# Optimization experiments

Hardware: AMD Instinct MI355X
Metric: run time of the kernel (lower is better)

The kernel has to match this reference:

```python
import jax, jax.numpy as jnp
import numpy as np

NUM_HEADS = 8

def setup_inputs() -> dict:
    key = jax.random.key(0)
    k1, k2, k3, k4 = jax.random.split(key, 4)
    B, N, C = 2, 4096, 768
    x = jax.random.normal(k1, (B, N, C), dtype=jnp.float32)
    w_qkv = jax.random.normal(k2, (C, 3 * C), dtype=jnp.float32) * (C ** -0.5)
    w_proj = jax.random.normal(k3, (C, C), dtype=jnp.float32) * (C ** -0.5)
    b_proj = jax.random.normal(k4, (C,), dtype=jnp.float32) * 0.02
    return {"x": x, "w_qkv": w_qkv, "w_proj": w_proj, "b_proj": b_proj}

def reference(x, w_qkv, w_proj, b_proj):
    B, N, C = x.shape
    H = NUM_HEADS
    Dh = C // H
    scale = Dh ** -0.5
    # qkv: [B, N, 3C] -> [B, N, 3, H, Dh] -> [3, B, H, N, Dh]
    qkv = (x @ w_qkv).reshape(B, N, 3, H, Dh).transpose(2, 0, 3, 1, 4)
    q, k, v = qkv[0], qkv[1], qkv[2]
    attn = jnp.einsum('bhqd,bhkd->bhqk', q, k) * scale  # [B,H,N,N]
    attn = jax.nn.softmax(attn, axis=-1)
    out = jnp.einsum('bhqk,bhkd->bhqd', attn, v)        # [B,H,N,Dh]
    out = out.transpose(0, 2, 1, 3).reshape(B, N, C)
    return out @ w_proj + b_proj
```

## Files before the change

kernel.cpp:

```cpp
#include <hip/hip_runtime.h>
#include <hip/hip_bf16.h>

typedef __attribute__((ext_vector_type(8))) short short8;
typedef __attribute__((ext_vector_type(4))) short short4v;
typedef __attribute__((ext_vector_type(4))) float f32x4;
typedef __attribute__((ext_vector_type(16))) float f32x16;

#define MFMA16(a,b,c) __builtin_amdgcn_mfma_f32_16x16x32_bf16(a,b,c,0,0,0)
#define MFMA32(a,b,c) __builtin_amdgcn_mfma_f32_32x32x16_bf16(a,b,c,0,0,0)

__device__ __forceinline__ unsigned short f2b_rne(float f){
  union { float f; unsigned int u; } v; v.f = f;
  unsigned int u = v.u;
  return (unsigned short)((u + 0x7FFFu + ((u >> 16) & 1u)) >> 16);
}

__device__ __forceinline__ f32x16 zero16(){
  f32x16 z;
  #pragma unroll
  for (int i = 0; i < 16; ++i) z[i] = 0.f;
  return z;
}

__global__ __launch_bounds__(256) void k_cvt(const float* __restrict__ in,
                                             unsigned short* __restrict__ out, int n8){
  int i = blockIdx.x * 256 + threadIdx.x;
  if (i >= n8) return;
  const float4* p = (const float4*)in + (size_t)i * 2;
  float4 a = p[0], b = p[1];
  short8 o;
  o[0] = (short)f2b_rne(a.x); o[1] = (short)f2b_rne(a.y);
  o[2] = (short)f2b_rne(a.z); o[3] = (short)f2b_rne(a.w);
  o[4] = (short)f2b_rne(b.x); o[5] = (short)f2b_rne(b.y);
  o[6] = (short)f2b_rne(b.z); o[7] = (short)f2b_rne(b.w);
  *((short8*)out + i) = o;
}

__global__ void k_transpose_cvt(const float* __restrict__ in, unsigned short* __restrict__ out,
                                int R, int Cc){
  __shared__ unsigned short tile[32][33];
  int c0 = blockIdx.x * 32, r0 = blockIdx.y * 32;
  int tx = threadIdx.x, ty = threadIdx.y;
  #pragma unroll
  for (int i = 0; i < 32; i += 8)
    tile[ty + i][tx] = f2b_rne(in[(size_t)(r0 + ty + i) * Cc + c0 + tx]);
  __syncthreads();
  #pragma unroll
  for (int i = 0; i < 32; i += 8)
    out[(size_t)(c0 + ty + i) * R + r0 + tx] = tile[tx][ty + i];
}

__global__ __launch_bounds__(256) void k_gemm_qkv(
    const unsigned short* __restrict__ A,
    const unsigned short* __restrict__ Bt,
    unsigned short* __restrict__ qbuf,
    unsigned short* __restrict__ kbuf,
    unsigned short* __restrict__ vtb)
{
  __shared__ short As[128 * 40];
  __shared__ short Bs[128 * 40];
  int m0 = blockIdx.x * 128, n0 = blockIdx.y * 128;
  int t = threadIdx.x, l = t & 63, w = t >> 6;
  int lr = l & 15, lh = l >> 4;
  int wr = w >> 1, wc = w & 1;

  int row0 = t >> 2, cs0 = t & 3;
  int row1 = row0 + 64;
  const unsigned short* ga0 = A  + (size_t)(m0 + row0) * 768 + cs0 * 8;
  const unsigned short* ga1 = A  + (size_t)(m0 + row1) * 768 + cs0 * 8;
  const unsigned short* gb0 = Bt + (size_t)(n0 + row0) * 768 + cs0 * 8;
  const unsigned short* gb1 = Bt + (size_t)(n0 + row1) * 768 + cs0 * 8;
  short* la0 = As + row0 * 40 + cs0 * 8;
  short* la1 = As + row1 * 40 + cs0 * 8;
  short* lb0 = Bs + row0 * 40 + cs0 * 8;
  short* lb1 = Bs + row1 * 40 + cs0 * 8;

  f32x4 acc[4][4];
  f32x4 z4 = {0.f, 0.f, 0.f, 0.f};
  #pragma unroll
  for (int mf = 0; mf < 4; ++mf)
    #pragma unroll
    for (int nf = 0; nf < 4; ++nf) acc[mf][nf] = z4;

  short8 ra0 = *(const short8*)ga0;
  short8 ra1 = *(const short8*)ga1;
  short8 rb0 = *(const short8*)gb0;
  short8 rb1 = *(const short8*)gb1;

  for (int kt = 0; kt < 24; ++kt){
    __syncthreads();
    *(short8*)la0 = ra0; *(short8*)la1 = ra1;
    *(short8*)lb0 = rb0; *(short8*)lb1 = rb1;
    __syncthreads();
    if (kt < 23){
      ra0 = *(const short8*)(ga0 + (kt + 1) * 32);
      ra1 = *(const short8*)(ga1 + (kt + 1) * 32);
      rb0 = *(const short8*)(gb0 + (kt + 1) * 32);
      rb1 = *(const short8*)(gb1 + (kt + 1) * 32);
    }
    short8 af[4], bfm[4];
    #pragma unroll
    for (int mf = 0; mf < 4; ++mf)
      af[mf] = *(const short8*)(As + (wr * 64 + mf * 16 + lr) * 40 + lh * 8);
    #pragma unroll
    for (int nf = 0; nf < 4; ++nf)
      bfm[nf] = *(const short8*)(Bs + (wc * 64 + nf * 16 + lr) * 40 + lh * 8);
    #pragma unroll
    for (int mf = 0; mf < 4; ++mf)
      #pragma unroll
      for (int nf = 0; nf < 4; ++nf)
        acc[mf][nf] = MFMA16(af[mf], bfm[nf], acc[mf][nf]);
  }

  const float qscale = 0.10206207261596577f * 1.4426950408889634f;
  int three = n0 / 768;
  int b_ = m0 >> 12;
  int ntok0 = m0 & 4095;
  #pragma unroll
  for (int nf = 0; nf < 4; ++nf){
    int gcol = n0 + wc * 64 + nf * 16 + lr;
    int jj = gcol - three * 768;
    int h = jj / 96;
    int dh = jj - h * 96;
    #pragma unroll
    for (int mf = 0; mf < 4; ++mf){
      int ntok = ntok0 + wr * 64 + mf * 16 + lh * 4;
      if (three == 0){
        unsigned short* dst = qbuf + (size_t)(b_ * 8 + h) * 4096 * 96;
        #pragma unroll
        for (int r = 0; r < 4; ++r)
          dst[(size_t)(ntok + r) * 96 + dh] = f2b_rne(acc[mf][nf][r] * qscale);
      } else if (three == 1){
        unsigned short* dst = kbuf + (size_t)(b_ * 8 + h) * 4096 * 96;
        #pragma unroll
        for (int r = 0; r < 4; ++r)
          dst[(size_t)(ntok + r) * 96 + dh] = f2b_rne(acc[mf][nf][r]);
      } else {
        short4v sv;
        #pragma unroll
        for (int r = 0; r < 4; ++r) sv[r] = (short)f2b_rne(acc[mf][nf][r]);
        *(short4v*)(vtb + ((size_t)(b_ * 8 + h) * 96 + dh) * 4096 + ntok) = sv;
      }
    }
  }
}

__global__ __launch_bounds__(512) __attribute__((amdgpu_waves_per_eu(4, 4)))
void k_attn7(
    const unsigned short* __restrict__ qb,
    const unsigned short* __restrict__ kb,
    const unsigned short* __restrict__ vtb,
    unsigned short* __restrict__ ao)
{
  __shared__ short lds[27136];
  const int bh = blockIdx.x;
  const int qt = blockIdx.y;
  const int tid = threadIdx.x;
  const int ln = tid & 63, wid = tid >> 6;
  const int qc = ln & 31, hi = ln >> 5;
  const int set = wid >> 2, qquad = wid & 3;
  const int q0 = qt * 128 + qquad * 32;

  const unsigned short* qbase = qb  + (size_t)bh * 4096 * 96;
  const unsigned short* kbase = kb  + (size_t)bh * 4096 * 96;
  const unsigned short* vbase = vtb + (size_t)bh * 96 * 4096;

  short8 qf[6];
  #pragma unroll
  for (int kw = 0; kw < 6; ++kw)
    qf[kw] = *(const short8*)(qbase + (size_t)(q0 + qc) * 96 + kw * 16 + hi * 8);

  int koff[3], loffK[3], voff[3], loffV[3];
  #pragma unroll
  for (int j = 0; j < 3; ++j){
    int ck = tid + j * 512;
    int s = (ck >= 768) ? 1 : 0;
    int cc = ck - s * 768;
    int r = cc / 12, cl = cc - r * 12;
    koff[j] = (s * 64 + r) * 96 + cl * 8;
    loffK[j] = s * 6656 + r * 104 + cl * 8;
  }
  #pragma unroll
  for (int j = 0; j < 3; ++j){
    int cv = tid + j * 512;
    int s = (cv >= 768) ? 1 : 0;
    int cc = cv - s * 768;
    int r = cc >> 3, cl = cc & 7;
    voff[j] = r * 4096 + s * 64 + cl * 8;
    loffV[j] = 13312 + s * 6912 + r * 72 + cl * 8;
  }

  short8 rsK[3], rsV[3];
  #pragma unroll
  for (int j = 0; j < 3; ++j){ rsK[j] = *(const short8*)(kbase + koff[j]); koff[j] += 12288; }
  #pragma unroll
  for (int j = 0; j < 3; ++j){ rsV[j] = *(const short8*)(vbase + voff[j]); voff[j] += 128; }
  #pragma unroll
  for (int j = 0; j < 3; ++j) *(short8*)(lds + loffK[j]) = rsK[j];
  #pragma unroll
  for (int j = 0; j < 3; ++j) *(short8*)(lds + loffV[j]) = rsV[j];

  f32x16 oacc[3];
  #pragma unroll
  for (int dt = 0; dt < 3; ++dt) oacc[dt] = zero16();
  float mr = -1e30f, lr_ = 0.f;

  const short* Kb = lds + set * 6656 + qc * 104 + hi * 8;
  const short* Vb = lds + 13312 + set * 6912 + qc * 72 + hi * 8;

#define CVTPK(d, lo_, hi_) asm("v_cvt_pk_bf16_f32 %0, %1, %2" : "=v"(d) : "v"(lo_), "v"(hi_))
#define PLSWAP(x_, y_)     asm("v_permlane32_swap_b32 %0, %1" : "+v"(x_), "+v"(y_))

#define PA_H(pa_, s_)                                                                    \
  {                                                                                      \
    unsigned int a_, b_;                                                                 \
    union { unsigned int u[4]; short8 s; } pk_;                                          \
    CVTPK(a_, s_[0],  s_[1]);  CVTPK(b_, s_[4],  s_[5]);  PLSWAP(a_, b_); pk_.u[0]=a_; pk_.u[2]=b_; \
    CVTPK(a_, s_[2],  s_[3]);  CVTPK(b_, s_[6],  s_[7]);  PLSWAP(a_, b_); pk_.u[1]=a_; pk_.u[3]=b_; \
    pa_[0] = pk_.s;                                                                      \
    CVTPK(a_, s_[8],  s_[9]);  CVTPK(b_, s_[12], s_[13]); PLSWAP(a_, b_); pk_.u[0]=a_; pk_.u[2]=b_; \
    CVTPK(a_, s_[10], s_[11]); CVTPK(b_, s_[14], s_[15]); PLSWAP(a_, b_); pk_.u[1]=a_; pk_.u[3]=b_; \
    pa_[1] = pk_.s;                                                                      \
  }

#define SOFTMAX_H(s_)                                                                    \
  {                                                                                      \
    float t0 = fmaxf(s_[0], s_[1]),  t1 = fmaxf(s_[2], s_[3]);                           \
    float t2 = fmaxf(s_[4], s_[5]),  t3 = fmaxf(s_[6], s_[7]);                           \
    t0 = fmaxf(t0, fmaxf(s_[8],  s_[9]));  t1 = fmaxf(t1, fmaxf(s_[10], s_[11]));        \
    t2 = fmaxf(t2, fmaxf(s_[12], s_[13])); t3 = fmaxf(t3, fmaxf(s_[14], s_[15]));        \
    float tmax = fmaxf(fmaxf(t0, t1), fmaxf(t2, t3));                                    \
    tmax = fmaxf(tmax, __shfl_xor(tmax, 32, 64));                                        \
    if (!__all(tmax - mr <= 8.0f)){                                                      \
      float mn = fmaxf(mr, tmax);                                                        \
      float al = exp2f(mr - mn);                                                         \
      _Pragma("unroll")                                                                  \
      for (int dt = 0; dt < 3; ++dt)                                                     \
        _Pragma("unroll")                                                                 \
        for (int r = 0; r < 16; ++r) oacc[dt][r] *= al;                                  \
      lr_ *= al; mr = mn;                                                                \
    }                                                                                    \
    float p0 = 0.f, p1 = 0.f, p2 = 0.f, p3 = 0.f;                                        \
    _Pragma("unroll")                                                                    \
    for (int r = 0; r < 16; r += 4){                                                     \
      s_[r]   = exp2f(s_[r]   - mr); p0 += s_[r];                                        \
      s_[r+1] = exp2f(s_[r+1] - mr); p1 += s_[r+1];                                      \
      s_[r+2] = exp2f(s_[r+2] - mr); p2 += s_[r+2];                                      \
      s_[r+3] = exp2f(s_[r+3] - mr); p3 += s_[r+3];                                      \
    }                                                                                    \
    float psum = (p0 + p1) + (p2 + p3);                                                  \
    psum += __shfl_xor(psum, 32, 64);                                                    \
    lr_ += psum;                                                                         \
  }

  for (int ss = 0; ss < 32; ++ss){
    __syncthreads();

    {
      f32x16 s0 = zero16();
      __builtin_amdgcn_s_setprio(1);
      #pragma unroll
      for (int kw = 0; kw < 6; ++kw){
        short8 kf = *(const short8*)(Kb + kw * 16);
        s0 = MFMA32(kf, qf[kw], s0);
      }
      __builtin_amdgcn_s_setprio(0);

      SOFTMAX_H(s0)
      short8 pa0[2];
      PA_H(pa0, s0)

      if (ss < 31){
        #pragma unroll
        for (int j = 0; j < 3; ++j){ rsK[j] = *(const short8*)(kbase + koff[j]); koff[j] += 12288; }
      }

      __builtin_amdgcn_s_setprio(1);
      #pragma unroll
      for (int dt = 0; dt < 3; ++dt){
        #pragma unroll
        for (int w = 0; w < 2; ++w){
          short8 vf = *(const short8*)(Vb + dt * 2304 + w * 16);
          oacc[dt] = MFMA32(vf, pa0[w], oacc[dt]);
        }
      }
      __builtin_amdgcn_s_setprio(0);
    }

    {
      f32x16 s0 = zero16();
      __builtin_amdgcn_s_setprio(1);
      #pragma unroll
      for (int kw = 0; kw < 6; ++kw){
        short8 kf = *(const short8*)(Kb + 3328 + kw * 16);
        s0 = MFMA32(kf, qf[kw], s0);
      }
      __builtin_amdgcn_s_setprio(0);

      SOFTMAX_H(s0)
      short8 pa0[2];
      PA_H(pa0, s0)

      if (ss < 31){
        #pragma unroll
        for (int j = 0; j < 3; ++j){ rsV[j] = *(const short8*)(vbase + voff[j]); voff[j] += 128; }
      }

      __builtin_amdgcn_s_setprio(1);
      #pragma unroll
      for (int dt = 0; dt < 3; ++dt){
        #pragma unroll
        for (int w = 0; w < 2; ++w){
          short8 vf = *(const short8*)(Vb + dt * 2304 + 32 + w * 16);
          oacc[dt] = MFMA32(vf, pa0[w], oacc[dt]);
        }
      }
      __builtin_amdgcn_s_setprio(0);
    }

    __syncthreads();
    if (ss < 31){
      #pragma unroll
      for (int j = 0; j < 3; ++j) *(short8*)(lds + loffK[j]) = rsK[j];
      #pragma unroll
      for (int j = 0; j < 3; ++j) *(short8*)(lds + loffV[j]) = rsV[j];
    }
  }

  float* fl = (float*)lds;
  {
    __syncthreads();
    if (set == 1){
      #pragma unroll
      for (int dt = 0; dt < 3; ++dt)
        #pragma unroll
        for (int r = 0; r < 16; ++r)
          fl[qquad * 3072 + dt * 1024 + r * 64 + ln] = oacc[dt][r];
      fl[12288 + qquad * 64 + ln] = mr;
      fl[12544 + qquad * 64 + ln] = lr_;
    }
    __syncthreads();
    if (set == 0){
      float m1v = fl[12288 + qquad * 64 + ln];
      float l1v = fl[12544 + qquad * 64 + ln];
      float M  = fmaxf(mr, m1v);
      float w0 = exp2f(mr - M), w1 = exp2f(m1v - M);
      lr_ = w0 * lr_ + w1 * l1v;
      #pragma unroll
      for (int dt = 0; dt < 3; ++dt)
        #pragma unroll
        for (int r = 0; r < 16; ++r)
          oacc[dt][r] = w0 * oacc[dt][r] + w1 * fl[qquad * 3072 + dt * 1024 + r * 64 + ln];
    }
  }

  if (set == 0){
    int b_ = bh >> 3, h = bh & 7;
    float inv = 1.0f / lr_;
    unsigned short* orow = ao + (size_t)(b_ * 4096 + q0 + qc) * 768 + h * 96;
    #pragma unroll
    for (int dt = 0; dt < 3; ++dt)
      #pragma unroll
      for (int g4 = 0; g4 < 4; ++g4){
        short4v sv;
        #pragma unroll
        for (int r = 0; r < 4; ++r) sv[r] = (short)f2b_rne(oacc[dt][g4 * 4 + r] * inv);
        *(short4v*)(orow + dt * 32 + g4 * 8 + hi * 4) = sv;
      }
  }
#undef CVTPK
#undef PLSWAP
#undef PA_H
#undef SOFTMAX_H
}

__global__ __launch_bounds__(256) void k_gemm_proj(
    const unsigned short* __restrict__ A,
    const unsigned short* __restrict__ Bt,
    const float* __restrict__ bias,
    float* __restrict__ out)
{
  __shared__ short As[128 * 40];
  __shared__ short Bs[128 * 40];
  int m0 = blockIdx.x * 128, n0 = blockIdx.y * 128;
  int t = threadIdx.x, l = t & 63, w = t >> 6;
  int lr = l & 15, lh = l >> 4;
  int wr = w >> 1, wc = w & 1;

  int row0 = t >> 2, cs0 = t & 3;
  int row1 = row0 + 64;
  const unsigned short* ga0 = A  + (size_t)(m0 + row0) * 768 + cs0 * 8;
  const unsigned short* ga1 = A  + (size_t)(m0 + row1) * 768 + cs0 * 8;
  const unsigned short* gb0 = Bt + (size_t)(n0 + row0) * 768 + cs0 * 8;
  const unsigned short* gb1 = Bt + (size_t)(n0 + row1) * 768 + cs0 * 8;
  short* la0 = As + row0 * 40 + cs0 * 8;
  short* la1 = As + row1 * 40 + cs0 * 8;
  short* lb0 = Bs + row0 * 40 + cs0 * 8;
  short* lb1 = Bs + row1 * 40 + cs0 * 8;

  f32x4 acc[4][4];
  f32x4 z4 = {0.f, 0.f, 0.f, 0.f};
  #pragma unroll
  for (int mf = 0; mf < 4; ++mf)
    #pragma unroll
    for (int nf = 0; nf < 4; ++nf) acc[mf][nf] = z4;

  short8 ra0 = *(const short8*)ga0;
  short8 ra1 = *(const short8*)ga1;
  short8 rb0 = *(const short8*)gb0;
  short8 rb1 = *(const short8*)gb1;

  for (int kt = 0; kt < 24; ++kt){
    __syncthreads();
    *(short8*)la0 = ra0; *(short8*)la1 = ra1;
    *(short8*)lb0 = rb0; *(short8*)lb1 = rb1;
    __syncthreads();
    if (kt < 23){
      ra0 = *(const short8*)(ga0 + (kt + 1) * 32);
      ra1 = *(const short8*)(ga1 + (kt + 1) * 32);
      rb0 = *(const short8*)(gb0 + (kt + 1) * 32);
      rb1 = *(const short8*)(gb1 + (kt + 1) * 32);
    }
    short8 af[4], bfm[4];
    #pragma unroll
    for (int mf = 0; mf < 4; ++mf)
      af[mf] = *(const short8*)(As + (wr * 64 + mf * 16 + lr) * 40 + lh * 8);
    #pragma unroll
    for (int nf = 0; nf < 4; ++nf)
      bfm[nf] = *(const short8*)(Bs + (wc * 64 + nf * 16 + lr) * 40 + lh * 8);
    #pragma unroll
    for (int mf = 0; mf < 4; ++mf)
      #pragma unroll
      for (int nf = 0; nf < 4; ++nf)
        acc[mf][nf] = MFMA16(af[mf], bfm[nf], acc[mf][nf]);
  }

  #pragma unroll
  for (int nf = 0; nf < 4; ++nf){
    int gcol = n0 + wc * 64 + nf * 16 + lr;
    float bb = bias[gcol];
    #pragma unroll
    for (int mf = 0; mf < 4; ++mf){
      int grow = m0 + wr * 64 + mf * 16 + lh * 4;
      #pragma unroll
      for (int r = 0; r < 4; ++r)
        out[(size_t)(grow + r) * 768 + gcol] = acc[mf][nf][r] + bb;
    }
  }
}

extern "C" void kernel_launch(void* const* d_in, const int* in_sizes, int n_in,
                              void* d_out, int out_size, void* d_ws, size_t ws_size,
                              hipStream_t stream) {
  const float* x      = (const float*)d_in[0];
  const float* w_qkv  = (const float*)d_in[1];
  const float* w_proj = (const float*)d_in[2];
  const float* b_proj = (const float*)d_in[3];
  float* out = (float*)d_out;
  char* ws = (char*)d_ws;

  unsigned short* xb     = (unsigned short*)(ws);
  unsigned short* wqkvt  = (unsigned short*)(ws + 12582912);
  unsigned short* wprojt = (unsigned short*)(ws + 16121856);
  unsigned short* qbuf   = (unsigned short*)(ws + 17301504);
  unsigned short* kbuf   = (unsigned short*)(ws + 29884416);
  unsigned short* vtb    = (unsigned short*)(ws + 42467328);
  unsigned short* aob    = xb;

  k_cvt<<<3072, 256, 0, stream>>>(x, xb, 786432);
  k_transpose_cvt<<<dim3(72, 24), dim3(32, 8), 0, stream>>>(w_qkv, wqkvt, 768, 2304);
  k_transpose_cvt<<<dim3(24, 24), dim3(32, 8), 0, stream>>>(w_proj, wprojt, 768, 768);
  k_gemm_qkv<<<dim3(64, 18), 256, 0, stream>>>(xb, wqkvt, qbuf, kbuf, vtb);
  k_attn7<<<dim3(16, 32), 512, 0, stream>>>(qbuf, kbuf, vtb, aob);
  k_gemm_proj<<<dim3(64, 6), 256, 0, stream>>>(aob, wprojt, b_proj, out);
}
```

Before: 236.1 us.

## Double-buffer K/V tiles in LDS and issue global prefetch before softmax

Doubles the attention kernel's LDS allocation so K/V tiles alternate between two buffers, which removes the second barrier per iteration. The global loads for the next tile now issue before the softmax rather than after it, so they overlap more compute. Occupancy hint drops from 4 to 2 waves per EU to match the larger LDS use, and the max reduction becomes a serial chain. Fewer resident waves may hurt latency hiding, and the bigger LDS footprint limits the number of blocks per CU.

```diff
diff --git a/kernel.cpp b/kernel.cpp
--- a/kernel.cpp
+++ b/kernel.cpp
@@ -145,14 +145,14 @@
   }
 }
 
-__global__ __launch_bounds__(512) __attribute__((amdgpu_waves_per_eu(4, 4)))
-void k_attn7(
+__global__ __launch_bounds__(512) __attribute__((amdgpu_waves_per_eu(2, 2)))
+void k_attn8(
     const unsigned short* __restrict__ qb,
     const unsigned short* __restrict__ kb,
     const unsigned short* __restrict__ vtb,
     unsigned short* __restrict__ ao)
 {
-  __shared__ short lds[27136];
+  __shared__ short lds[54272];
   const int bh = blockIdx.x;
   const int qt = blockIdx.y;
   const int tid = threadIdx.x;
@@ -205,8 +205,8 @@
   for (int dt = 0; dt < 3; ++dt) oacc[dt] = zero16();
   float mr = -1e30f, lr_ = 0.f;
 
-  const short* Kb = lds + set * 6656 + qc * 104 + hi * 8;
-  const short* Vb = lds + 13312 + set * 6912 + qc * 72 + hi * 8;
+  const short* KbL = lds + set * 6656 + qc * 104 + hi * 8;
+  const short* VbL = lds + 13312 + set * 6912 + qc * 72 + hi * 8;
 
 #define CVTPK(d, lo_, hi_) asm("v_cvt_pk_bf16_f32 %0, %1, %2" : "=v"(d) : "v"(lo_), "v"(hi_))
 #define PLSWAP(x_, y_)     asm("v_permlane32_swap_b32 %0, %1" : "+v"(x_), "+v"(y_))
@@ -225,14 +225,17 @@
 
 #define SOFTMAX_H(s_)                                                                    \
   {                                                                                      \
-    float t0 = fmaxf(s_[0], s_[1]),  t1 = fmaxf(s_[2], s_[3]);                           \
-    float t2 = fmaxf(s_[4], s_[5]),  t3 = fmaxf(s_[6], s_[7]);                           \
-    t0 = fmaxf(t0, fmaxf(s_[8],  s_[9]));  t1 = fmaxf(t1, fmaxf(s_[10], s_[11]));        \
-    t2 = fmaxf(t2, fmaxf(s_[12], s_[13])); t3 = fmaxf(t3, fmaxf(s_[14], s_[15]));        \
-    float tmax = fmaxf(fmaxf(t0, t1), fmaxf(t2, t3));                                    \
-    tmax = fmaxf(tmax, __shfl_xor(tmax, 32, 64));                                        \
-    if (!__all(tmax - mr <= 8.0f)){                                                      \
-      float mn = fmaxf(mr, tmax);                                                        \
+    float tm = fmaxf(s_[0], s_[1]);                                                      \
+    tm = fmaxf(fmaxf(tm, s_[2]),  s_[3]);                                                \
+    tm = fmaxf(fmaxf(tm, s_[4]),  s_[5]);                                                \
+    tm = fmaxf(fmaxf(tm, s_[6]),  s_[7]);                                                \
+    tm = fmaxf(fmaxf(tm, s_[8]),  s_[9]);                                                \
+    tm = fmaxf(fmaxf(tm, s_[10]), s_[11]);                                               \
+    tm = fmaxf(fmaxf(tm, s_[12]), s_[13]);                                               \
+    tm = fmaxf(fmaxf(tm, s_[14]), s_[15]);                                               \
+    tm = fmaxf(tm, __shfl_xor(tm, 32, 64));                                              \
+    if (!__all(tm - mr <= 8.0f)){                                                        \
+      float mn = fmaxf(mr, tm);                                                          \
       float al = exp2f(mr - mn);                                                         \
       _Pragma("unroll")                                                                  \
       for (int dt = 0; dt < 3; ++dt)                                                     \
@@ -255,6 +258,9 @@
 
   for (int ss = 0; ss < 32; ++ss){
     __syncthreads();
+    const int cb = (ss & 1) * 27136;
+    const short* Kb = KbL + cb;
+    const short* Vb = VbL + cb;
 
     {
       f32x16 s0 = zero16();
@@ -266,14 +272,14 @@
       }
       __builtin_amdgcn_s_setprio(0);
 
+      if (ss < 31){
+        #pragma unroll
+        for (int j = 0; j < 3; ++j){ rsK[j] = *(const short8*)(kbase + koff[j]); koff[j] += 12288; }
+      }
+
       SOFTMAX_H(s0)
       short8 pa0[2];
       PA_H(pa0, s0)
-
-      if (ss < 31){
-        #pragma unroll
-        for (int j = 0; j < 3; ++j){ rsK[j] = *(const short8*)(kbase + koff[j]); koff[j] += 12288; }
-      }
 
       __builtin_amdgcn_s_setprio(1);
       #pragma unroll
@@ -297,14 +303,14 @@
       }
       __builtin_amdgcn_s_setprio(0);
 
+      if (ss < 31){
+        #pragma unroll
+        for (int j = 0; j < 3; ++j){ rsV[j] = *(const short8*)(vbase + voff[j]); voff[j] += 128; }
+      }
+
       SOFTMAX_H(s0)
       short8 pa0[2];
       PA_H(pa0, s0)
-
-      if (ss < 31){
-        #pragma unroll
-        for (int j = 0; j < 3; ++j){ rsV[j] = *(const short8*)(vbase + voff[j]); voff[j] += 128; }
-      }
 
       __builtin_amdgcn_s_setprio(1);
       #pragma unroll
@@ -318,12 +324,12 @@
       __builtin_amdgcn_s_setprio(0);
     }
 
-    __syncthreads();
     if (ss < 31){
-      #pragma unroll
-      for (int j = 0; j < 3; ++j) *(short8*)(lds + loffK[j]) = rsK[j];
-      #pragma unroll
-      for (int j = 0; j < 3; ++j) *(short8*)(lds + loffV[j]) = rsV[j];
+      const int nb = ((ss & 1) ^ 1) * 27136;
+      #pragma unroll
+      for (int j = 0; j < 3; ++j) *(short8*)(lds + nb + loffK[j]) = rsK[j];
+      #pragma unroll
+      for (int j = 0; j < 3; ++j) *(short8*)(lds + nb + loffV[j]) = rsV[j];
     }
   }
 
@@ -471,6 +477,6 @@
   k_transpose_cvt<<<dim3(72, 24), dim3(32, 8), 0, stream>>>(w_qkv, wqkvt, 768, 2304);
   k_transpose_cvt<<<dim3(24, 24), dim3(32, 8), 0, stream>>>(w_proj, wprojt, 768, 768);
   k_gemm_qkv<<<dim3(64, 18), 256, 0, stream>>>(xb, wqkvt, qbuf, kbuf, vtb);
-  k_attn7<<<dim3(16, 32), 512, 0, stream>>>(qbuf, kbuf, vtb, aob);
+  k_attn8<<<dim3(16, 32), 512, 0, stream>>>(qbuf, kbuf, vtb, aob);
   k_gemm_proj<<<dim3(64, 6), 256, 0, stream>>>(aob, wprojt, b_proj, out);
 }
```

Measured after the change: 232.9 us. Within noise of the previous version (-1.3%).
